# Performance work log

Measured on AMD Instinct MI355X. Metric: run time of the kernel, lower is better.

Reference implementation:

```python
import jax, jax.numpy as jnp
import numpy as np

B, T, C = 4, 2048, 1024
H, D = 16, 64
SCALE = D ** -0.5


def setup_inputs() -> dict:
    key = jax.random.key(0)
    ks = jax.random.split(key, 5)
    s = 0.02
    return {
        "hidden_states": jax.random.normal(ks[0], (B, T, C), dtype=jnp.float32),
        "attention_mask": jnp.ones((B, T), dtype=jnp.int32),
        "Wq": jax.random.normal(ks[1], (C, H * D), dtype=jnp.float32) * s,
        "Wk": jax.random.normal(ks[2], (C, H * D), dtype=jnp.float32) * s,
        "Wv": jax.random.normal(ks[3], (C, H * D), dtype=jnp.float32) * s,
        "Wo": jax.random.normal(ks[4], (H * D, C), dtype=jnp.float32) * s,
        "bo": jnp.zeros((C,), dtype=jnp.float32),
    }


def reference(hidden_states, attention_mask, Wq, Wk, Wv, Wo, bo):
    b, t, _ = hidden_states.shape
    # projections -> (B, H, T, D)
    q = (hidden_states @ Wq).reshape(b, t, H, D).transpose(0, 2, 1, 3)
    k = (hidden_states @ Wk).reshape(b, t, H, D).transpose(0, 2, 1, 3)
    v = (hidden_states @ Wv).reshape(b, t, H, D).transpose(0, 2, 1, 3)
    # scores (B, H, Tq, Tk)
    scores = jnp.einsum("bhqd,bhkd->bhqk", q, k) * SCALE
    mask = attention_mask[:, None, None, :]  # (B,1,1,T), dim==2 branch
    scores = jnp.where(mask == 0, -jnp.inf, scores)
    probs = jax.nn.softmax(scores, axis=-1)
    out = jnp.einsum("bhqk,bhkd->bhqd", probs, v)
    out = out.transpose(0, 2, 1, 3).reshape(b, t, H * D)
    return out @ Wo + bo
```

## Files before the change

kernel.cpp:

```cpp
#include <hip/hip_runtime.h>
#include <hip/hip_bf16.h>

#define B_ 4
#define T_ 2048
#define C_ 1024
#define H_ 16
#define D_ 64
#define SCALE_ 0.125f
#define L2E 1.4426950408889634f
#define SE (SCALE_ * L2E)

typedef __attribute__((ext_vector_type(8))) short bf16x8;
typedef __attribute__((ext_vector_type(4))) float f32x4;

__device__ __forceinline__ unsigned short f2bf(float f) {
    union { float f; unsigned u; } v; v.f = f;
    unsigned r = v.u + 0x7fff + ((v.u >> 16) & 1);
    return (unsigned short)(r >> 16);
}

__device__ __forceinline__ unsigned pk2bf(float a, float b) {
    __hip_bfloat162 t = __float22bfloat162_rn(make_float2(a, b));
    union { __hip_bfloat162 h; unsigned u; } c; c.h = t;
    return c.u;
}

__device__ __forceinline__ void gl_lds16(const unsigned short* g, unsigned short* l) {
    __builtin_amdgcn_global_load_lds(
        (const __attribute__((address_space(1))) void*)g,
        (__attribute__((address_space(3))) void*)l,
        16, 0, 0);
}

__global__ void cvtw_kernel(const float4* __restrict__ in, ushort4* __restrict__ out,
                            const float* __restrict__ Wq, const float* __restrict__ Wk,
                            const float* __restrict__ Wv, const float* __restrict__ Wo,
                            unsigned short* __restrict__ Wqkv_t, unsigned short* __restrict__ Wo_t) {
    __shared__ float tile[64][65];
    const int bid = blockIdx.x;
    const int t = threadIdx.x;
    if (bid < 8192) {
        int i = bid * 256 + t;
        float4 v = in[i];
        ushort4 o;
        o.x = f2bf(v.x); o.y = f2bf(v.y); o.z = f2bf(v.z); o.w = f2bf(v.w);
        out[i] = o;
        return;
    }
    const int wb = bid - 8192;
    const int mtx = wb >> 8;
    const float* W = (mtx == 0) ? Wq : (mtx == 1) ? Wk : (mtx == 2) ? Wv : Wo;
    unsigned short* Out = (mtx < 3) ? (Wqkv_t + (size_t)mtx * 1024 * 1024) : Wo_t;
    const int tl = wb & 255;
    const int tx = tl & 15, ty = tl >> 4;
    const int col = t & 63, rb = t >> 6;
#pragma unroll
    for (int rr = 0; rr < 16; ++rr) {
        int r = rb * 16 + rr;
        tile[r][col] = W[(size_t)(ty * 64 + r) * 1024 + tx * 64 + col];
    }
    __syncthreads();
#pragma unroll
    for (int rr = 0; rr < 16; ++rr) {
        int r = rb * 16 + rr;
        Out[(size_t)(tx * 64 + r) * 1024 + ty * 64 + col] = f2bf(tile[col][r]);
    }
}

__global__ __launch_bounds__(256) void gemm_qkv_kernel(
    const unsigned short* __restrict__ A, const unsigned short* __restrict__ Bt,
    unsigned short* __restrict__ Qg, unsigned short* __restrict__ Kf, unsigned short* __restrict__ Vf) {
    __shared__ __align__(16) unsigned short As[128 * 64];
    __shared__ __align__(16) unsigned short Bs[128 * 64];
    const int tid = threadIdx.x;
    const int w = tid >> 6, lane = tid & 63;
    const int quad = lane >> 4, l16 = lane & 15;
    const int m0 = blockIdx.y * 128, n0 = blockIdx.x * 128;
    const int mw = (w >> 1) * 64, nw = (w & 1) * 64;
    const int K = 1024;
    const int srow = lane >> 3;
    const int scol = (lane & 7) * 8;

    const f32x4 fzero = {0.f, 0.f, 0.f, 0.f};
    f32x4 acc[4][4];
#pragma unroll
    for (int i = 0; i < 4; ++i)
#pragma unroll
        for (int j = 0; j < 4; ++j) acc[i][j] = fzero;

#pragma unroll 1
    for (int k0 = 0; k0 < K; k0 += 64) {
#pragma unroll
        for (int g = 0; g < 4; ++g) {
            gl_lds16(A + (size_t)(m0 + w * 32 + g * 8 + srow) * K + k0 + scol,  As + (w * 32 + g * 8) * 64);
            gl_lds16(Bt + (size_t)(n0 + w * 32 + g * 8 + srow) * K + k0 + scol, Bs + (w * 32 + g * 8) * 64);
        }
        __syncthreads();
#pragma unroll
        for (int ks = 0; ks < 2; ++ks) {
            bf16x8 a[4], b[4];
#pragma unroll
            for (int i = 0; i < 4; ++i)
                a[i] = *(const bf16x8*)(As + (mw + i * 16 + l16) * 64 + ks * 32 + quad * 8);
#pragma unroll
            for (int j = 0; j < 4; ++j)
                b[j] = *(const bf16x8*)(Bs + (nw + j * 16 + l16) * 64 + ks * 32 + quad * 8);
#pragma unroll
            for (int i = 0; i < 4; ++i)
#pragma unroll
                for (int j = 0; j < 4; ++j)
                    acc[i][j] = __builtin_amdgcn_mfma_f32_16x16x32_bf16(a[i], b[j], acc[i][j], 0, 0, 0);
        }
        __syncthreads();
    }

#pragma unroll
    for (int j = 0; j < 4; ++j) {
        int gn = n0 + nw + j * 16 + l16;
        int tensor = gn >> 10;
        int nl = gn & 1023;
        int hh = nl >> 6, dd = nl & 63;
#pragma unroll
        for (int i = 0; i < 4; ++i) {
            int gmb = m0 + mw + i * 16 + quad * 4;
            int bb = gmb >> 11;
            size_t bhh = (size_t)(bb * 16 + hh);
            if (tensor == 0) {
#pragma unroll
                for (int r = 0; r < 4; ++r) {
                    int tt = (gmb + r) & 2047;
                    Qg[(bhh * 2048 + tt) * 64 + dd] = f2bf(acc[i][j][r] * SE);
                }
            } else if (tensor == 1) {
#pragma unroll
                for (int r = 0; r < 4; ++r) {
                    int tt = (gmb + r) & 2047;
                    Kf[bhh * 131072 + (size_t)(tt >> 4) * 1024 + (dd >> 5) * 512 +
                       (((dd >> 3) & 3) * 16 + (tt & 15)) * 8 + (dd & 7)] = f2bf(acc[i][j][r]);
                }
            } else {
                int tt = gmb & 2047;
                ushort4 v4;
                v4.x = f2bf(acc[i][j][0]); v4.y = f2bf(acc[i][j][1]);
                v4.z = f2bf(acc[i][j][2]); v4.w = f2bf(acc[i][j][3]);
                *(ushort4*)(Vf + bhh * 131072 + (size_t)(tt >> 5) * 2048 + (dd >> 4) * 512 +
                            (((tt >> 3) & 3) * 16 + (dd & 15)) * 8 + (tt & 7)) = v4;
            }
        }
    }
}

__device__ __forceinline__ void attn_step_staged(
    int k0, const unsigned short* Kc, const unsigned short* Vc,
    unsigned short* Kn, unsigned short* Vn, int kn0,
    const unsigned short* __restrict__ Kg, const unsigned short* __restrict__ Vg,
    unsigned short* Pw, const bf16x8 (&aq)[2][2], const bf16x8& vones,
    f32x4 (&po)[2][4], f32x4 (&pl)[2],
    const int* __restrict__ mrow, int w, int lane, int quad, int l16) {

    gl_lds16(Kg + (size_t)(kn0 >> 4) * 1024 + w * 512 + lane * 8, Kn + w * 512);
    gl_lds16(Vg + (size_t)(kn0 >> 5) * 2048 + w * 512 + lane * 8, Vn + w * 512);

    bf16x8 ka0[4], ka1[4];
#pragma unroll
    for (int kt = 0; kt < 4; ++kt) {
        ka0[kt] = *(const bf16x8*)(Kc + kt * 1024 + lane * 8);
        ka1[kt] = *(const bf16x8*)(Kc + kt * 1024 + 512 + lane * 8);
    }

    const f32x4 fzero = {0.f, 0.f, 0.f, 0.f};
    int mk = mrow[k0 + lane];
    bool allok = (__ballot(mk != 0) == 0xFFFFFFFFFFFFFFFFull);

    if (allok) {
#pragma unroll
        for (int kt = 0; kt < 4; ++kt) {
            int pidx = ((((kt & 1) << 1) | (quad >> 1)) * 16 + l16) * 8 + (quad & 1) * 4;
#pragma unroll
            for (int qi = 0; qi < 2; ++qi) {
                f32x4 st = __builtin_amdgcn_mfma_f32_16x16x32_bf16(ka0[kt], aq[qi][0], fzero, 0, 0, 0);
                st = __builtin_amdgcn_mfma_f32_16x16x32_bf16(ka1[kt], aq[qi][1], st, 0, 0, 0);
                float p0 = __builtin_amdgcn_exp2f(st[0]);
                float p1 = __builtin_amdgcn_exp2f(st[1]);
                float p2 = __builtin_amdgcn_exp2f(st[2]);
                float p3 = __builtin_amdgcn_exp2f(st[3]);
                uint2 pk; pk.x = pk2bf(p0, p1); pk.y = pk2bf(p2, p3);
                *(uint2*)(Pw + (qi * 2 + (kt >> 1)) * 512 + pidx) = pk;
            }
        }
    } else {
#pragma unroll
        for (int kt = 0; kt < 4; ++kt) {
            int4 mv = *(const int4*)(mrow + k0 + kt * 16 + quad * 4);
            float mb0 = mv.x ? 0.f : -1e30f;
            float mb1 = mv.y ? 0.f : -1e30f;
            float mb2 = mv.z ? 0.f : -1e30f;
            float mb3 = mv.w ? 0.f : -1e30f;
            int pidx = ((((kt & 1) << 1) | (quad >> 1)) * 16 + l16) * 8 + (quad & 1) * 4;
#pragma unroll
            for (int qi = 0; qi < 2; ++qi) {
                f32x4 st = __builtin_amdgcn_mfma_f32_16x16x32_bf16(ka0[kt], aq[qi][0], fzero, 0, 0, 0);
                st = __builtin_amdgcn_mfma_f32_16x16x32_bf16(ka1[kt], aq[qi][1], st, 0, 0, 0);
                float p0 = __builtin_amdgcn_exp2f(st[0] + mb0);
                float p1 = __builtin_amdgcn_exp2f(st[1] + mb1);
                float p2 = __builtin_amdgcn_exp2f(st[2] + mb2);
                float p3 = __builtin_amdgcn_exp2f(st[3] + mb3);
                uint2 pk; pk.x = pk2bf(p0, p1); pk.y = pk2bf(p2, p3);
                *(uint2*)(Pw + (qi * 2 + (kt >> 1)) * 512 + pidx) = pk;
            }
        }
    }

    bf16x8 bv[2][4];
#pragma unroll
    for (int c = 0; c < 2; ++c)
#pragma unroll
        for (int nd = 0; nd < 4; ++nd)
            bv[c][nd] = *(const bf16x8*)(Vc + c * 2048 + nd * 512 + lane * 8);

    asm volatile("s_waitcnt lgkmcnt(0)" ::: "memory");

#pragma unroll
    for (int c = 0; c < 2; ++c)
#pragma unroll
        for (int qi = 0; qi < 2; ++qi) {
            bf16x8 ap = *(const bf16x8*)(Pw + (qi * 2 + c) * 512 + lane * 8);
#pragma unroll
            for (int nd = 0; nd < 4; ++nd)
                po[qi][nd] = __builtin_amdgcn_mfma_f32_16x16x32_bf16(ap, bv[c][nd], po[qi][nd], 0, 0, 0);
            pl[qi] = __builtin_amdgcn_mfma_f32_16x16x32_bf16(ap, vones, pl[qi], 0, 0, 0);
        }
}

__global__ __launch_bounds__(512, 4) void attn_kernel(
    const unsigned short* __restrict__ Qg, const unsigned short* __restrict__ Kf,
    const unsigned short* __restrict__ Vf, const int* __restrict__ mask,
    unsigned short* __restrict__ AO) {
    __shared__ __align__(16) unsigned short KsA[4096], KsB[4096];
    __shared__ __align__(16) unsigned short VsA[4096], VsB[4096];
    __shared__ __align__(16) unsigned short Pbuf[8][2048];

    const int tid = threadIdx.x;
    const int w = tid >> 6, lane = tid & 63;
    const int quad = lane >> 4, l16 = lane & 15;
    const int bid = blockIdx.x;
    const int bh = (bid & 7) * 8 + ((bid >> 6) & 7);
    const int qt = (bid >> 3) & 7;
    const int b = bh >> 4, h = bh & 15;
    const size_t bh_td = (size_t)bh * (2048 * 64);
    const int q0w = qt * 256 + w * 32;

    bf16x8 aq[2][2];
#pragma unroll
    for (int qi = 0; qi < 2; ++qi)
#pragma unroll
        for (int hh = 0; hh < 2; ++hh)
            aq[qi][hh] = *(const bf16x8*)(Qg + bh_td + (size_t)(q0w + qi * 16 + l16) * 64 + hh * 32 + quad * 8);

    const unsigned short* Kg = Kf + bh_td;
    const unsigned short* Vg = Vf + bh_td;
    const int* mrow = mask + b * 2048;

    bf16x8 vones;
#pragma unroll
    for (int i = 0; i < 8; ++i) vones[i] = (short)0x3F80;

    const f32x4 fzero = {0.f, 0.f, 0.f, 0.f};
    f32x4 po[2][4];
    f32x4 pl[2];
#pragma unroll
    for (int qi = 0; qi < 2; ++qi) {
        pl[qi] = fzero;
#pragma unroll
        for (int nd = 0; nd < 4; ++nd) po[qi][nd] = fzero;
    }

    gl_lds16(Kg + w * 512 + lane * 8, KsA + w * 512);
    gl_lds16(Vg + w * 512 + lane * 8, VsA + w * 512);
    asm volatile("s_waitcnt vmcnt(0)" ::: "memory");
    __syncthreads();

#pragma unroll 1
    for (int k0 = 0; k0 < 2048; k0 += 128) {
        attn_step_staged(k0, KsA, VsA, KsB, VsB, k0 + 64,
                         Kg, Vg, Pbuf[w], aq, vones, po, pl, mrow, w, lane, quad, l16);
        asm volatile("s_waitcnt vmcnt(0)" ::: "memory");
        __syncthreads();
        attn_step_staged(k0 + 64, KsB, VsB, KsA, VsA, (k0 + 128) & 2047,
                         Kg, Vg, Pbuf[w], aq, vones, po, pl, mrow, w, lane, quad, l16);
        asm volatile("s_waitcnt vmcnt(0)" ::: "memory");
        __syncthreads();
    }

#pragma unroll
    for (int qi = 0; qi < 2; ++qi)
#pragma unroll
        for (int r = 0; r < 4; ++r) {
            float linv = __builtin_amdgcn_rcpf(pl[qi][r]);
            int q = q0w + qi * 16 + quad * 4 + r;
            size_t ob = (size_t)(b * 2048 + q) * 1024 + h * 64;
#pragma unroll
            for (int nd = 0; nd < 4; ++nd)
                AO[ob + nd * 16 + l16] = f2bf(po[qi][nd][r] * linv);
        }
}

__global__ __launch_bounds__(256) void gemm_out_kernel(
    const unsigned short* __restrict__ A, const unsigned short* __restrict__ Bt,
    const float* __restrict__ bo, float* __restrict__ out) {
    __shared__ __align__(16) unsigned short As[128 * 64];
    __shared__ __align__(16) unsigned short Bs[128 * 64];
    const int tid = threadIdx.x;
    const int w = tid >> 6, lane = tid & 63;
    const int quad = lane >> 4, l16 = lane & 15;
    const int m0 = blockIdx.y * 128, n0 = blockIdx.x * 128;
    const int mw = (w >> 1) * 64, nw = (w & 1) * 64;
    const int K = 1024;
    const int srow = lane >> 3;
    const int scol = (lane & 7) * 8;

    const f32x4 fzero = {0.f, 0.f, 0.f, 0.f};
    f32x4 acc[4][4];
#pragma unroll
    for (int i = 0; i < 4; ++i)
#pragma unroll
        for (int j = 0; j < 4; ++j) acc[i][j] = fzero;

#pragma unroll 1
    for (int k0 = 0; k0 < K; k0 += 64) {
#pragma unroll
        for (int g = 0; g < 4; ++g) {
            gl_lds16(A + (size_t)(m0 + w * 32 + g * 8 + srow) * K + k0 + scol,  As + (w * 32 + g * 8) * 64);
            gl_lds16(Bt + (size_t)(n0 + w * 32 + g * 8 + srow) * K + k0 + scol, Bs + (w * 32 + g * 8) * 64);
        }
        __syncthreads();
#pragma unroll
        for (int ks = 0; ks < 2; ++ks) {
            bf16x8 a[4], b[4];
#pragma unroll
            for (int i = 0; i < 4; ++i)
                a[i] = *(const bf16x8*)(As + (mw + i * 16 + l16) * 64 + ks * 32 + quad * 8);
#pragma unroll
            for (int j = 0; j < 4; ++j)
                b[j] = *(const bf16x8*)(Bs + (nw + j * 16 + l16) * 64 + ks * 32 + quad * 8);
#pragma unroll
            for (int i = 0; i < 4; ++i)
#pragma unroll
                for (int j = 0; j < 4; ++j)
                    acc[i][j] = __builtin_amdgcn_mfma_f32_16x16x32_bf16(a[i], b[j], acc[i][j], 0, 0, 0);
        }
        __syncthreads();
    }

#pragma unroll
    for (int j = 0; j < 4; ++j) {
        int gn = n0 + nw + j * 16 + l16;
        float bias = bo[gn];
#pragma unroll
        for (int i = 0; i < 4; ++i) {
            int gmb = m0 + mw + i * 16 + quad * 4;
#pragma unroll
            for (int r = 0; r < 4; ++r)
                out[(size_t)(gmb + r) * 1024 + gn] = acc[i][j][r] + bias;
        }
    }
}

extern "C" void kernel_launch(void* const* d_in, const int* in_sizes, int n_in,
                              void* d_out, int out_size, void* d_ws, size_t ws_size,
                              hipStream_t stream) {
    const float* hs  = (const float*)d_in[0];
    const int* mask  = (const int*)d_in[1];
    const float* Wq  = (const float*)d_in[2];
    const float* Wk  = (const float*)d_in[3];
    const float* Wv  = (const float*)d_in[4];
    const float* Wo  = (const float*)d_in[5];
    const float* bo  = (const float*)d_in[6];
    float* out = (float*)d_out;

    char* ws = (char*)d_ws;
    unsigned short* hs_bf = (unsigned short*)(ws);
    unsigned short* wqkv  = (unsigned short*)(ws + 16777216);
    unsigned short* wo_t  = (unsigned short*)(ws + 23068672);
    unsigned short* Qg    = (unsigned short*)(ws + 25165824);
    unsigned short* Kf    = (unsigned short*)(ws + 41943040);
    unsigned short* Vf    = (unsigned short*)(ws + 58720256);
    unsigned short* AO    = (unsigned short*)(ws + 75497472);

    cvtw_kernel<<<9216, 256, 0, stream>>>((const float4*)hs, (ushort4*)hs_bf,
                                          Wq, Wk, Wv, Wo, wqkv, wo_t);
    gemm_qkv_kernel<<<dim3(24, 64), 256, 0, stream>>>(hs_bf, wqkv, Qg, Kf, Vf);
    attn_kernel<<<512, 512, 0, stream>>>(Qg, Kf, Vf, mask, AO);
    gemm_out_kernel<<<dim3(8, 64), 256, 0, stream>>>(AO, wo_t, bo, out);
}
```

Measured before the change: 281.7 us.

## Rewrite QKV GEMM as 256x256 pipelined tile with swizzled LDS, shrink out-GEMM K-step

The QKV projection GEMM moves from 128x128 tiles with 256 threads to 256x256 tiles with 512 threads. It uses a double-buffered, XOR-swizzled LDS layout (128 KB), a prefetch schedule split into phases with explicit vmcnt waits and raw s_barrier, s_setprio around the MFMA blocks, and a block-index swizzle for L2 locality. The intent is to overlap global loads with MFMA work, cut LDS bank conflicts and raise data reuse per tile. Separately, the output GEMM's K step drops from 64 to 32 with a smaller LDS footprint, and its loop is no longer forced un-unrolled. The risks are register pressure from the 8x4 accumulators, lower occupancy, and fragile hand-written wait counts.

```diff
diff --git a/kernel.cpp b/kernel.cpp
--- a/kernel.cpp
+++ b/kernel.cpp
@@ -30,6 +30,10 @@
         (const __attribute__((address_space(1))) void*)g,
         (__attribute__((address_space(3))) void*)l,
         16, 0, 0);
+}
+
+__device__ __forceinline__ void bar_fence() {
+    asm volatile("s_barrier" ::: "memory");
 }
 
 __global__ void cvtw_kernel(const float4* __restrict__ in, ushort4* __restrict__ out,
@@ -67,82 +71,140 @@
     }
 }
 
-__global__ __launch_bounds__(256) void gemm_qkv_kernel(
+__device__ __forceinline__ void qkv_stage_half(
+    const unsigned short* __restrict__ A, const unsigned short* __restrict__ Bt,
+    unsigned short* Lsh, int S, int m0, int n0, int tid, int w) {
+    const int ks = S >> 2, part = S & 3;
+    const int isB = part & 1, h = part >> 1;
+    const unsigned short* G = isB ? Bt : A;
+    const int row0 = (isB ? n0 : m0) + h * 128;
+    const int ldsb = (isB ? 32768 : 0) + ((ks & 1) * 2 + h) * 8192;
+#pragma unroll
+    for (int i = 0; i < 2; ++i) {
+        int idx = i * 512 + tid;
+        int r = idx >> 3;
+        int c2 = ((idx & 7) * 16) ^ ((r & 7) << 4);
+        gl_lds16(G + (size_t)(row0 + r) * 1024 + ks * 64 + (c2 >> 1),
+                 Lsh + ldsb + (i * 512 + w * 64) * 8);
+    }
+}
+
+template <int PH>
+__device__ __forceinline__ void qkv_phase(
+    int kt, const unsigned short* __restrict__ A, const unsigned short* __restrict__ Bt,
+    unsigned short* Lsh, f32x4 (&acc)[8][4],
+    int m0, int n0, int tid, int w, int wr, int wc, int quad, int l16) {
+    const int slot = kt & 1;
+    const int Mh = PH >> 1, Nh = PH & 1;
+    const int abase = (slot * 2 + Mh) * 8192;
+    const int bbase = 32768 + (slot * 2 + Nh) * 8192;
+
+    bf16x8 a[4][2], b[2][2];
+#pragma unroll
+    for (int i2 = 0; i2 < 4; ++i2) {
+        int r = wr * 64 + i2 * 16 + l16;
+#pragma unroll
+        for (int ks = 0; ks < 2; ++ks) {
+            int cb = (ks * 64 + quad * 16) ^ ((r & 7) << 4);
+            a[i2][ks] = *(const bf16x8*)(Lsh + abase + r * 64 + (cb >> 1));
+        }
+    }
+#pragma unroll
+    for (int j2 = 0; j2 < 2; ++j2) {
+        int r = wc * 32 + j2 * 16 + l16;
+#pragma unroll
+        for (int ks = 0; ks < 2; ++ks) {
+            int cb = (ks * 64 + quad * 16) ^ ((r & 7) << 4);
+            b[j2][ks] = *(const bf16x8*)(Lsh + bbase + r * 64 + (cb >> 1));
+        }
+    }
+
+    {
+        int S = kt * 4 + PH + 6;
+        if (S < 64) qkv_stage_half(A, Bt, Lsh, S, m0, n0, tid, w);
+    }
+
+    bar_fence();
+    __builtin_amdgcn_s_setprio(1);
+#pragma unroll
+    for (int i2 = 0; i2 < 4; ++i2)
+#pragma unroll
+        for (int j2 = 0; j2 < 2; ++j2)
+#pragma unroll
+            for (int ks = 0; ks < 2; ++ks)
+                acc[Mh * 4 + i2][Nh * 2 + j2] = __builtin_amdgcn_mfma_f32_16x16x32_bf16(
+                    a[i2][ks], b[j2][ks], acc[Mh * 4 + i2][Nh * 2 + j2], 0, 0, 0);
+    __builtin_amdgcn_s_setprio(0);
+
+    if (PH == 3) {
+        if (kt == 14) asm volatile("s_waitcnt vmcnt(0)" ::: "memory");
+        else          asm volatile("s_waitcnt vmcnt(4)" ::: "memory");
+    }
+    bar_fence();
+}
+
+__global__ __launch_bounds__(512, 2) void gemm_qkv_kernel(
     const unsigned short* __restrict__ A, const unsigned short* __restrict__ Bt,
     unsigned short* __restrict__ Qg, unsigned short* __restrict__ Kf, unsigned short* __restrict__ Vf) {
-    __shared__ __align__(16) unsigned short As[128 * 64];
-    __shared__ __align__(16) unsigned short Bs[128 * 64];
+    __shared__ __align__(16) unsigned short Lsh[65536];
+
     const int tid = threadIdx.x;
     const int w = tid >> 6, lane = tid & 63;
     const int quad = lane >> 4, l16 = lane & 15;
-    const int m0 = blockIdx.y * 128, n0 = blockIdx.x * 128;
-    const int mw = (w >> 1) * 64, nw = (w & 1) * 64;
-    const int K = 1024;
-    const int srow = lane >> 3;
-    const int scol = (lane & 7) * 8;
+    const int wr = w >> 2, wc = w & 3;
+    const int bid = blockIdx.x;
+    const int swz = (bid & 7) * 48 + (bid >> 3);
+    const int m0 = (swz & 31) * 256, n0 = (swz >> 5) * 256;
 
     const f32x4 fzero = {0.f, 0.f, 0.f, 0.f};
-    f32x4 acc[4][4];
-#pragma unroll
-    for (int i = 0; i < 4; ++i)
+    f32x4 acc[8][4];
+#pragma unroll
+    for (int i = 0; i < 8; ++i)
 #pragma unroll
         for (int j = 0; j < 4; ++j) acc[i][j] = fzero;
 
-#pragma unroll 1
-    for (int k0 = 0; k0 < K; k0 += 64) {
-#pragma unroll
-        for (int g = 0; g < 4; ++g) {
-            gl_lds16(A + (size_t)(m0 + w * 32 + g * 8 + srow) * K + k0 + scol,  As + (w * 32 + g * 8) * 64);
-            gl_lds16(Bt + (size_t)(n0 + w * 32 + g * 8 + srow) * K + k0 + scol, Bs + (w * 32 + g * 8) * 64);
-        }
-        __syncthreads();
-#pragma unroll
-        for (int ks = 0; ks < 2; ++ks) {
-            bf16x8 a[4], b[4];
-#pragma unroll
-            for (int i = 0; i < 4; ++i)
-                a[i] = *(const bf16x8*)(As + (mw + i * 16 + l16) * 64 + ks * 32 + quad * 8);
-#pragma unroll
-            for (int j = 0; j < 4; ++j)
-                b[j] = *(const bf16x8*)(Bs + (nw + j * 16 + l16) * 64 + ks * 32 + quad * 8);
-#pragma unroll
-            for (int i = 0; i < 4; ++i)
-#pragma unroll
-                for (int j = 0; j < 4; ++j)
-                    acc[i][j] = __builtin_amdgcn_mfma_f32_16x16x32_bf16(a[i], b[j], acc[i][j], 0, 0, 0);
-        }
-        __syncthreads();
-    }
-
-#pragma unroll
-    for (int j = 0; j < 4; ++j) {
-        int gn = n0 + nw + j * 16 + l16;
+#pragma unroll
+    for (int S = 0; S < 6; ++S) qkv_stage_half(A, Bt, Lsh, S, m0, n0, tid, w);
+    asm volatile("s_waitcnt vmcnt(4)" ::: "memory");
+    bar_fence();
+
+#pragma unroll 2
+    for (int kt = 0; kt < 16; ++kt) {
+        qkv_phase<0>(kt, A, Bt, Lsh, acc, m0, n0, tid, w, wr, wc, quad, l16);
+        qkv_phase<1>(kt, A, Bt, Lsh, acc, m0, n0, tid, w, wr, wc, quad, l16);
+        qkv_phase<2>(kt, A, Bt, Lsh, acc, m0, n0, tid, w, wr, wc, quad, l16);
+        qkv_phase<3>(kt, A, Bt, Lsh, acc, m0, n0, tid, w, wr, wc, quad, l16);
+    }
+
+#pragma unroll
+    for (int nj = 0; nj < 4; ++nj) {
+        int gn = n0 + (nj >> 1) * 128 + wc * 32 + (nj & 1) * 16 + l16;
         int tensor = gn >> 10;
         int nl = gn & 1023;
         int hh = nl >> 6, dd = nl & 63;
 #pragma unroll
-        for (int i = 0; i < 4; ++i) {
-            int gmb = m0 + mw + i * 16 + quad * 4;
+        for (int mi = 0; mi < 8; ++mi) {
+            int gmb = m0 + (mi >> 2) * 128 + wr * 64 + (mi & 3) * 16 + quad * 4;
             int bb = gmb >> 11;
             size_t bhh = (size_t)(bb * 16 + hh);
             if (tensor == 0) {
 #pragma unroll
                 for (int r = 0; r < 4; ++r) {
                     int tt = (gmb + r) & 2047;
-                    Qg[(bhh * 2048 + tt) * 64 + dd] = f2bf(acc[i][j][r] * SE);
+                    Qg[(bhh * 2048 + tt) * 64 + dd] = f2bf(acc[mi][nj][r] * SE);
                 }
             } else if (tensor == 1) {
 #pragma unroll
                 for (int r = 0; r < 4; ++r) {
                     int tt = (gmb + r) & 2047;
                     Kf[bhh * 131072 + (size_t)(tt >> 4) * 1024 + (dd >> 5) * 512 +
-                       (((dd >> 3) & 3) * 16 + (tt & 15)) * 8 + (dd & 7)] = f2bf(acc[i][j][r]);
+                       (((dd >> 3) & 3) * 16 + (tt & 15)) * 8 + (dd & 7)] = f2bf(acc[mi][nj][r]);
                 }
             } else {
                 int tt = gmb & 2047;
                 ushort4 v4;
-                v4.x = f2bf(acc[i][j][0]); v4.y = f2bf(acc[i][j][1]);
-                v4.z = f2bf(acc[i][j][2]); v4.w = f2bf(acc[i][j][3]);
+                v4.x = f2bf(acc[mi][nj][0]); v4.y = f2bf(acc[mi][nj][1]);
+                v4.z = f2bf(acc[mi][nj][2]); v4.w = f2bf(acc[mi][nj][3]);
                 *(ushort4*)(Vf + bhh * 131072 + (size_t)(tt >> 5) * 2048 + (dd >> 4) * 512 +
                             (((tt >> 3) & 3) * 16 + (dd & 15)) * 8 + (tt & 7)) = v4;
             }
@@ -308,16 +370,16 @@
 __global__ __launch_bounds__(256) void gemm_out_kernel(
     const unsigned short* __restrict__ A, const unsigned short* __restrict__ Bt,
     const float* __restrict__ bo, float* __restrict__ out) {
-    __shared__ __align__(16) unsigned short As[128 * 64];
-    __shared__ __align__(16) unsigned short Bs[128 * 64];
+    __shared__ __align__(16) unsigned short As[128 * 32];
+    __shared__ __align__(16) unsigned short Bs[128 * 32];
     const int tid = threadIdx.x;
     const int w = tid >> 6, lane = tid & 63;
     const int quad = lane >> 4, l16 = lane & 15;
     const int m0 = blockIdx.y * 128, n0 = blockIdx.x * 128;
     const int mw = (w >> 1) * 64, nw = (w & 1) * 64;
     const int K = 1024;
-    const int srow = lane >> 3;
-    const int scol = (lane & 7) * 8;
+    const int srow = lane >> 2;
+    const int scol = (lane & 3) * 8;
 
     const f32x4 fzero = {0.f, 0.f, 0.f, 0.f};
     f32x4 acc[4][4];
@@ -326,29 +388,24 @@
 #pragma unroll
         for (int j = 0; j < 4; ++j) acc[i][j] = fzero;
 
-#pragma unroll 1
-    for (int k0 = 0; k0 < K; k0 += 64) {
-#pragma unroll
-        for (int g = 0; g < 4; ++g) {
-            gl_lds16(A + (size_t)(m0 + w * 32 + g * 8 + srow) * K + k0 + scol,  As + (w * 32 + g * 8) * 64);
-            gl_lds16(Bt + (size_t)(n0 + w * 32 + g * 8 + srow) * K + k0 + scol, Bs + (w * 32 + g * 8) * 64);
-        }
+    for (int k0 = 0; k0 < K; k0 += 32) {
+        gl_lds16(A + (size_t)(m0 + w * 32 + srow) * K + k0 + scol,       As + (w * 32) * 32);
+        gl_lds16(A + (size_t)(m0 + w * 32 + 16 + srow) * K + k0 + scol,  As + (w * 32 + 16) * 32);
+        gl_lds16(Bt + (size_t)(n0 + w * 32 + srow) * K + k0 + scol,      Bs + (w * 32) * 32);
+        gl_lds16(Bt + (size_t)(n0 + w * 32 + 16 + srow) * K + k0 + scol, Bs + (w * 32 + 16) * 32);
         __syncthreads();
-#pragma unroll
-        for (int ks = 0; ks < 2; ++ks) {
-            bf16x8 a[4], b[4];
-#pragma unroll
-            for (int i = 0; i < 4; ++i)
-                a[i] = *(const bf16x8*)(As + (mw + i * 16 + l16) * 64 + ks * 32 + quad * 8);
+        bf16x8 a[4], b[4];
+#pragma unroll
+        for (int i = 0; i < 4; ++i)
+            a[i] = *(const bf16x8*)(As + (mw + i * 16 + l16) * 32 + quad * 8);
+#pragma unroll
+        for (int j = 0; j < 4; ++j)
+            b[j] = *(const bf16x8*)(Bs + (nw + j * 16 + l16) * 32 + quad * 8);
+#pragma unroll
+        for (int i = 0; i < 4; ++i)
 #pragma unroll
             for (int j = 0; j < 4; ++j)
-                b[j] = *(const bf16x8*)(Bs + (nw + j * 16 + l16) * 64 + ks * 32 + quad * 8);
-#pragma unroll
-            for (int i = 0; i < 4; ++i)
-#pragma unroll
-                for (int j = 0; j < 4; ++j)
-                    acc[i][j] = __builtin_amdgcn_mfma_f32_16x16x32_bf16(a[i], b[j], acc[i][j], 0, 0, 0);
-        }
+                acc[i][j] = __builtin_amdgcn_mfma_f32_16x16x32_bf16(a[i], b[j], acc[i][j], 0, 0, 0);
         __syncthreads();
     }
 
@@ -389,7 +446,7 @@
 
     cvtw_kernel<<<9216, 256, 0, stream>>>((const float4*)hs, (ushort4*)hs_bf,
                                           Wq, Wk, Wv, Wo, wqkv, wo_t);
-    gemm_qkv_kernel<<<dim3(24, 64), 256, 0, stream>>>(hs_bf, wqkv, Qg, Kf, Vf);
+    gemm_qkv_kernel<<<384, 512, 0, stream>>>(hs_bf, wqkv, Qg, Kf, Vf);
     attn_kernel<<<512, 512, 0, stream>>>(Qg, Kf, Vf, mask, AO);
     gemm_out_kernel<<<dim3(8, 64), 256, 0, stream>>>(AO, wo_t, bo, out);
 }
```

Result: no change. 284.0 us (+0.8%).

## Double-buffer swizzled QKV GEMM with larger tiles; shrink out-GEMM K-step

Applied to the files above, without the earlier changes.

The QKV projection GEMM becomes a 512-thread kernel with 128x256 tiles. It double-buffers LDS with an XOR-swizzled layout, prefetching the next K tile while MFMAs run on the current one. It also remaps block IDs for L2 locality and raises wave priority around the MFMA block. Separately, the output GEMM drops to a K-step of 32 with half-size LDS buffers, which means twice as many barriers. These changes aim to hide global-load latency and cut LDS bank conflicts, at the cost of more LDS per block (96 KB) and possibly lower occupancy.

```diff
diff --git a/kernel.cpp b/kernel.cpp
--- a/kernel.cpp
+++ b/kernel.cpp
@@ -30,6 +30,10 @@
         (const __attribute__((address_space(1))) void*)g,
         (__attribute__((address_space(3))) void*)l,
         16, 0, 0);
+}
+
+__device__ __forceinline__ void bar_fence() {
+    asm volatile("s_barrier" ::: "memory");
 }
 
 __global__ void cvtw_kernel(const float4* __restrict__ in, ushort4* __restrict__ out,
@@ -67,19 +71,44 @@
     }
 }
 
-__global__ __launch_bounds__(256) void gemm_qkv_kernel(
+__device__ __forceinline__ void qkv_stage_A(
+    const unsigned short* __restrict__ A, unsigned short* Lsh,
+    int slot, int kt, int m0, int tid, int w) {
+#pragma unroll
+    for (int i = 0; i < 2; ++i) {
+        int idx = i * 512 + tid;
+        int r = idx >> 3;
+        int c2 = ((idx & 7) * 16) ^ ((r & 7) << 4);
+        gl_lds16(A + (size_t)(m0 + r) * 1024 + kt * 64 + (c2 >> 1),
+                 Lsh + slot * 8192 + (i * 512 + w * 64) * 8);
+    }
+}
+
+__device__ __forceinline__ void qkv_stage_B(
+    const unsigned short* __restrict__ Bt, unsigned short* Lsh,
+    int slot, int kt, int n0, int tid, int w) {
+#pragma unroll
+    for (int i = 0; i < 4; ++i) {
+        int idx = i * 512 + tid;
+        int r = idx >> 3;
+        int c2 = ((idx & 7) * 16) ^ ((r & 7) << 4);
+        gl_lds16(Bt + (size_t)(n0 + r) * 1024 + kt * 64 + (c2 >> 1),
+                 Lsh + 16384 + slot * 16384 + (i * 512 + w * 64) * 8);
+    }
+}
+
+__global__ __launch_bounds__(512, 2) void gemm_qkv_kernel(
     const unsigned short* __restrict__ A, const unsigned short* __restrict__ Bt,
     unsigned short* __restrict__ Qg, unsigned short* __restrict__ Kf, unsigned short* __restrict__ Vf) {
-    __shared__ __align__(16) unsigned short As[128 * 64];
-    __shared__ __align__(16) unsigned short Bs[128 * 64];
+    __shared__ __align__(16) unsigned short Lsh[49152];
+
     const int tid = threadIdx.x;
     const int w = tid >> 6, lane = tid & 63;
     const int quad = lane >> 4, l16 = lane & 15;
-    const int m0 = blockIdx.y * 128, n0 = blockIdx.x * 128;
-    const int mw = (w >> 1) * 64, nw = (w & 1) * 64;
-    const int K = 1024;
-    const int srow = lane >> 3;
-    const int scol = (lane & 7) * 8;
+    const int wr = w >> 2, wc = w & 3;
+    const int bid = blockIdx.x;
+    const int swz = (bid & 7) * 96 + (bid >> 3);
+    const int m0 = (swz & 63) * 128, n0 = (swz >> 6) * 256;
 
     const f32x4 fzero = {0.f, 0.f, 0.f, 0.f};
     f32x4 acc[4][4];
@@ -88,41 +117,53 @@
 #pragma unroll
         for (int j = 0; j < 4; ++j) acc[i][j] = fzero;
 
+    qkv_stage_A(A, Lsh, 0, 0, m0, tid, w);
+    qkv_stage_B(Bt, Lsh, 0, 0, n0, tid, w);
+    asm volatile("s_waitcnt vmcnt(0)" ::: "memory");
+    bar_fence();
+
 #pragma unroll 1
-    for (int k0 = 0; k0 < K; k0 += 64) {
-#pragma unroll
-        for (int g = 0; g < 4; ++g) {
-            gl_lds16(A + (size_t)(m0 + w * 32 + g * 8 + srow) * K + k0 + scol,  As + (w * 32 + g * 8) * 64);
-            gl_lds16(Bt + (size_t)(n0 + w * 32 + g * 8 + srow) * K + k0 + scol, Bs + (w * 32 + g * 8) * 64);
-        }
-        __syncthreads();
+    for (int kt = 0; kt < 16; ++kt) {
+        const int slot = kt & 1;
+        qkv_stage_A(A, Lsh, slot ^ 1, (kt + 1) & 15, m0, tid, w);
+        qkv_stage_B(Bt, Lsh, slot ^ 1, (kt + 1) & 15, n0, tid, w);
+
 #pragma unroll
         for (int ks = 0; ks < 2; ++ks) {
             bf16x8 a[4], b[4];
 #pragma unroll
-            for (int i = 0; i < 4; ++i)
-                a[i] = *(const bf16x8*)(As + (mw + i * 16 + l16) * 64 + ks * 32 + quad * 8);
-#pragma unroll
-            for (int j = 0; j < 4; ++j)
-                b[j] = *(const bf16x8*)(Bs + (nw + j * 16 + l16) * 64 + ks * 32 + quad * 8);
+            for (int i = 0; i < 4; ++i) {
+                int r = wr * 64 + i * 16 + l16;
+                int cb = (ks * 64 + quad * 16) ^ ((r & 7) << 4);
+                a[i] = *(const bf16x8*)(Lsh + slot * 8192 + r * 64 + (cb >> 1));
+            }
+#pragma unroll
+            for (int j = 0; j < 4; ++j) {
+                int r = wc * 64 + j * 16 + l16;
+                int cb = (ks * 64 + quad * 16) ^ ((r & 7) << 4);
+                b[j] = *(const bf16x8*)(Lsh + 16384 + slot * 16384 + r * 64 + (cb >> 1));
+            }
+            __builtin_amdgcn_s_setprio(1);
 #pragma unroll
             for (int i = 0; i < 4; ++i)
 #pragma unroll
                 for (int j = 0; j < 4; ++j)
                     acc[i][j] = __builtin_amdgcn_mfma_f32_16x16x32_bf16(a[i], b[j], acc[i][j], 0, 0, 0);
-        }
-        __syncthreads();
+            __builtin_amdgcn_s_setprio(0);
+        }
+        asm volatile("s_waitcnt vmcnt(0)" ::: "memory");
+        bar_fence();
     }
 
 #pragma unroll
     for (int j = 0; j < 4; ++j) {
-        int gn = n0 + nw + j * 16 + l16;
+        int gn = n0 + wc * 64 + j * 16 + l16;
         int tensor = gn >> 10;
         int nl = gn & 1023;
         int hh = nl >> 6, dd = nl & 63;
 #pragma unroll
         for (int i = 0; i < 4; ++i) {
-            int gmb = m0 + mw + i * 16 + quad * 4;
+            int gmb = m0 + wr * 64 + i * 16 + quad * 4;
             int bb = gmb >> 11;
             size_t bhh = (size_t)(bb * 16 + hh);
             if (tensor == 0) {
@@ -308,16 +349,16 @@
 __global__ __launch_bounds__(256) void gemm_out_kernel(
     const unsigned short* __restrict__ A, const unsigned short* __restrict__ Bt,
     const float* __restrict__ bo, float* __restrict__ out) {
-    __shared__ __align__(16) unsigned short As[128 * 64];
-    __shared__ __align__(16) unsigned short Bs[128 * 64];
+    __shared__ __align__(16) unsigned short As[128 * 32];
+    __shared__ __align__(16) unsigned short Bs[128 * 32];
     const int tid = threadIdx.x;
     const int w = tid >> 6, lane = tid & 63;
     const int quad = lane >> 4, l16 = lane & 15;
     const int m0 = blockIdx.y * 128, n0 = blockIdx.x * 128;
     const int mw = (w >> 1) * 64, nw = (w & 1) * 64;
     const int K = 1024;
-    const int srow = lane >> 3;
-    const int scol = (lane & 7) * 8;
+    const int srow = lane >> 2;
+    const int scol = (lane & 3) * 8;
 
     const f32x4 fzero = {0.f, 0.f, 0.f, 0.f};
     f32x4 acc[4][4];
@@ -326,29 +367,24 @@
 #pragma unroll
         for (int j = 0; j < 4; ++j) acc[i][j] = fzero;
 
-#pragma unroll 1
-    for (int k0 = 0; k0 < K; k0 += 64) {
-#pragma unroll
-        for (int g = 0; g < 4; ++g) {
-            gl_lds16(A + (size_t)(m0 + w * 32 + g * 8 + srow) * K + k0 + scol,  As + (w * 32 + g * 8) * 64);
-            gl_lds16(Bt + (size_t)(n0 + w * 32 + g * 8 + srow) * K + k0 + scol, Bs + (w * 32 + g * 8) * 64);
-        }
+    for (int k0 = 0; k0 < K; k0 += 32) {
+        gl_lds16(A + (size_t)(m0 + w * 32 + srow) * K + k0 + scol,       As + (w * 32) * 32);
+        gl_lds16(A + (size_t)(m0 + w * 32 + 16 + srow) * K + k0 + scol,  As + (w * 32 + 16) * 32);
+        gl_lds16(Bt + (size_t)(n0 + w * 32 + srow) * K + k0 + scol,      Bs + (w * 32) * 32);
+        gl_lds16(Bt + (size_t)(n0 + w * 32 + 16 + srow) * K + k0 + scol, Bs + (w * 32 + 16) * 32);
         __syncthreads();
-#pragma unroll
-        for (int ks = 0; ks < 2; ++ks) {
-            bf16x8 a[4], b[4];
-#pragma unroll
-            for (int i = 0; i < 4; ++i)
-                a[i] = *(const bf16x8*)(As + (mw + i * 16 + l16) * 64 + ks * 32 + quad * 8);
+        bf16x8 a[4], b[4];
+#pragma unroll
+        for (int i = 0; i < 4; ++i)
+            a[i] = *(const bf16x8*)(As + (mw + i * 16 + l16) * 32 + quad * 8);
+#pragma unroll
+        for (int j = 0; j < 4; ++j)
+            b[j] = *(const bf16x8*)(Bs + (nw + j * 16 + l16) * 32 + quad * 8);
+#pragma unroll
+        for (int i = 0; i < 4; ++i)
 #pragma unroll
             for (int j = 0; j < 4; ++j)
-                b[j] = *(const bf16x8*)(Bs + (nw + j * 16 + l16) * 64 + ks * 32 + quad * 8);
-#pragma unroll
-            for (int i = 0; i < 4; ++i)
-#pragma unroll
-                for (int j = 0; j < 4; ++j)
-                    acc[i][j] = __builtin_amdgcn_mfma_f32_16x16x32_bf16(a[i], b[j], acc[i][j], 0, 0, 0);
-        }
+                acc[i][j] = __builtin_amdgcn_mfma_f32_16x16x32_bf16(a[i], b[j], acc[i][j], 0, 0, 0);
         __syncthreads();
     }
 
@@ -389,7 +425,7 @@
 
     cvtw_kernel<<<9216, 256, 0, stream>>>((const float4*)hs, (ushort4*)hs_bf,
                                           Wq, Wk, Wv, Wo, wqkv, wo_t);
-    gemm_qkv_kernel<<<dim3(24, 64), 256, 0, stream>>>(hs_bf, wqkv, Qg, Kf, Vf);
+    gemm_qkv_kernel<<<768, 512, 0, stream>>>(hs_bf, wqkv, Qg, Kf, Vf);
     attn_kernel<<<512, 512, 0, stream>>>(Qg, Kf, Vf, mask, AO);
     gemm_out_kernel<<<dim3(8, 64), 256, 0, stream>>>(AO, wo_t, bo, out);
 }
```

New measurement: 270.5 us. 1.04x faster.
